# Kernel tuning notes

Measured on AMD Instinct MI355X. Metric: run time of the kernel, lower is better.

## Reference

```python
import jax, jax.numpy as jnp
import numpy as np

H = 2048      # hidden_size
NH = 16       # num_heads
HD = H // NH  # attention_head_size = 128
NEG_BIAS = -10000.0


def setup_inputs() -> dict:
    key = jax.random.key(0)
    k1, k2, k3, k4, k5 = jax.random.split(key, 5)
    B, S = 2, 2048
    hidden_states = jax.random.normal(k1, (B, S, H), dtype=jnp.float32)
    scale = 1.0 / np.sqrt(H)
    w_qkv = jax.random.normal(k2, (H, 3 * H), dtype=jnp.float32) * scale
    b_qkv = jax.random.normal(k3, (3 * H,), dtype=jnp.float32) * 0.01
    w_out = jax.random.normal(k4, (H, H), dtype=jnp.float32) * scale
    b_out = jax.random.normal(k5, (H,), dtype=jnp.float32) * 0.01
    return {"hidden_states": hidden_states, "w_qkv": w_qkv, "b_qkv": b_qkv,
            "w_out": w_out, "b_out": b_out}


def reference(hidden_states, w_qkv, b_qkv, w_out, b_out):
    B, S, _ = hidden_states.shape
    # fused QKV projection -> [B, S, 3H]
    qkv = hidden_states @ w_qkv + b_qkv
    # split heads with 3*head_dim per head, then chunk (matches torch code)
    qkv = qkv.reshape(B, S, NH, 3 * HD).transpose(0, 2, 1, 3)  # [B, NH, S, 3*HD]
    q, k, v = jnp.split(qkv, 3, axis=-1)                       # each [B, NH, S, HD]
    # scaled scores [B, NH, S, S]
    scores = jnp.einsum('bhqd,bhkd->bhqk', q, k) / np.sqrt(HD)
    causal = jnp.tril(jnp.ones((S, S), dtype=bool))
    scores = jnp.where(causal[None, None], scores, jnp.float32(NEG_BIAS))
    probs = jax.nn.softmax(scores, axis=-1)
    ctx = jnp.einsum('bhqk,bhkd->bhqd', probs, v)  # [B, NH, S, HD]
    ctx = ctx.transpose(0, 2, 1, 3).reshape(B, S, H)
    return ctx @ w_out + b_out
```

## Files before the change

kernel.cpp:

```cpp
#include <hip/hip_runtime.h>
#include <hip/hip_bf16.h>

typedef __bf16 bf16x8 __attribute__((ext_vector_type(8)));
typedef float  f32x4  __attribute__((ext_vector_type(4)));

constexpr int   Bb   = 2;
constexpr int   Slen = 2048;
constexpr int   Hdim = 2048;
constexpr int   NHn  = 16;
constexpr int   HDd  = 128;
constexpr int   LDP  = 136;
constexpr float QSCALE = 0.08838834764831845f;
constexpr float NEG    = -1e30f;

__device__ __forceinline__ void gld16(const __bf16* g, __bf16* l) {
    __builtin_amdgcn_global_load_lds(
        (__attribute__((address_space(1))) void*)(uintptr_t)(const void*)g,
        (__attribute__((address_space(3))) void*)l, 16, 0, 0);
}

__global__ __launch_bounds__(256) void cvt_bf16(const float* __restrict__ in,
                                                __bf16* __restrict__ out) {
    const size_t i = (size_t)(blockIdx.x * 256 + threadIdx.x) * 8;
    f32x4 a = *(const f32x4*)(in + i), b = *(const f32x4*)(in + i + 4);
    bf16x8 r;
    r[0] = (__bf16)a[0]; r[1] = (__bf16)a[1]; r[2] = (__bf16)a[2]; r[3] = (__bf16)a[3];
    r[4] = (__bf16)b[0]; r[5] = (__bf16)b[1]; r[6] = (__bf16)b[2]; r[7] = (__bf16)b[3];
    *(bf16x8*)(out + i) = r;
}

__global__ __launch_bounds__(256) void transpose_cvt(const float* __restrict__ in,
                                                     __bf16* __restrict__ out,
                                                     int R, int C) {
    __shared__ float t[64][65];
    const int c0 = blockIdx.x * 64, r0 = blockIdx.y * 64;
    const int tx = threadIdx.x & 63, ty = threadIdx.x >> 6;
#pragma unroll
    for (int i = 0; i < 16; ++i) {
        int r = i * 4 + ty;
        t[r][tx] = in[(size_t)(r0 + r) * C + c0 + tx];
    }
    __syncthreads();
#pragma unroll
    for (int i = 0; i < 16; ++i) {
        int r = i * 4 + ty;
        out[(size_t)(c0 + r) * R + r0 + tx] = (__bf16)t[tx][r];
    }
}


#define BAR    __builtin_amdgcn_s_barrier()
#define LGKM0  asm volatile("s_waitcnt lgkmcnt(0)" ::: "memory")
#define VMC(n) asm volatile("s_waitcnt vmcnt(" #n ")" ::: "memory")

#define STAGE(op, half, tt)                                                          \
  do {                                                                               \
    const int tt_ = (tt);                                                            \
    if (tt_ < NT) {                                                                  \
      __bf16* dst_ = lds + ((tt_ & 1) << 15) + ((op) << 14) + ((half) << 13);        \
      const __bf16* src_ = (op) ? Bt : A;                                            \
      const int rb_ = (op) ? n0 : m0;                                               \
      const int k0_ = tt_ << 6;                                                      \
      _Pragma("unroll")                                                              \
      for (int i_ = 0; i_ < 2; ++i_) {                                               \
        const int c_  = (i_ << 9) + tid;                                             \
        const int rl_ = c_ >> 3;                                                     \
        const int grow_ = rb_ + ((op) ? (((rl_ >> 5) << 6) + ((half) << 5) + (rl_ & 31)) \
                                      : (((rl_ >> 6) << 7) + ((half) << 6) + (rl_ & 63))); \
        const int gk_ = k0_ + (((c_ & 7) ^ (rl_ & 7)) << 3);                         \
        gld16(src_ + (size_t)grow_ * Kdim + gk_, dst_ + (c_ << 3));                  \
      }                                                                              \
    }                                                                                \
  } while (0)

#define LDA(bufv, mh)                                                                \
  do {                                                                               \
    const __bf16* Ab_ = lds + ((bufv) << 15) + ((mh) << 13) + (wg << 12) + (l16 << 6); \
    _Pragma("unroll")                                                                \
    for (int q_ = 0; q_ < 4; ++q_)                                                   \
      _Pragma("unroll")                                                              \
      for (int kk_ = 0; kk_ < 2; ++kk_)                                              \
        af[q_][kk_] = *(const bf16x8*)(Ab_ + (q_ << 10) +                            \
                        ((((kk_ << 2) + quad) ^ (l16 & 7)) << 3));                   \
  } while (0)

#define LDB(bufv, nh)                                                                \
  do {                                                                               \
    const __bf16* Bb_ = lds + ((bufv) << 15) + 16384 + ((nh) << 13) + (gn << 11) + (l16 << 6); \
    _Pragma("unroll")                                                                \
    for (int q_ = 0; q_ < 2; ++q_)                                                   \
      _Pragma("unroll")                                                              \
      for (int kk_ = 0; kk_ < 2; ++kk_)                                              \
        bfr[((nh) << 1) + q_][kk_] = *(const bf16x8*)(Bb_ + (q_ << 10) +             \
                        ((((kk_ << 2) + quad) ^ (l16 & 7)) << 3));                   \
  } while (0)

#define MM(mh, nh)                                                                   \
  do {                                                                               \
    _Pragma("unroll")                                                                \
    for (int q_ = 0; q_ < 4; ++q_)                                                   \
      _Pragma("unroll")                                                              \
      for (int n_ = 0; n_ < 2; ++n_)                                                 \
        _Pragma("unroll")                                                            \
        for (int kk_ = 0; kk_ < 2; ++kk_)                                            \
          acc[((mh) << 2) + q_][((nh) << 1) + n_] =                                  \
            __builtin_amdgcn_mfma_f32_16x16x32_bf16(                                 \
              af[q_][kk_], bfr[((nh) << 1) + n_][kk_],                               \
              acc[((mh) << 2) + q_][((nh) << 1) + n_], 0, 0, 0);                     \
  } while (0)

template <int MODE>
__global__ __launch_bounds__(512, 2) void gemm8(
    const __bf16* __restrict__ A, const __bf16* __restrict__ Bt,
    const float* __restrict__ bias, int Kdim, int Ndim,
    float* __restrict__ Cout,
    __bf16* __restrict__ Qo, __bf16* __restrict__ Ko, __bf16* __restrict__ Vto) {
    __shared__ __bf16 lds[65536];
    const int tid  = threadIdx.x;
    const int lane = tid & 63, wave = tid >> 6;
    const int quad = lane >> 4, l16 = lane & 15;
    const int wg = wave >> 2;
    const int gn = wave & 3;
    const int m0 = blockIdx.y * 256, n0 = blockIdx.x * 256;
    const int NT = Kdim >> 6;

    f32x4  acc[8][4] = {};
    bf16x8 af[4][2];
    bf16x8 bfr[4][2];

    STAGE(0, 0, 0); STAGE(1, 0, 0); STAGE(1, 1, 0); STAGE(0, 1, 0);
    STAGE(0, 0, 1); STAGE(1, 0, 1); STAGE(1, 1, 1);
    VMC(6);
    BAR;

    for (int t = 0; t < NT; ++t) {
        const int cb = t & 1;
        LDA(cb, 0); LDB(cb, 0);
        STAGE(0, 1, t + 1);
        BAR; LGKM0;
        __builtin_amdgcn_s_setprio(1); MM(0, 0); __builtin_amdgcn_s_setprio(0);
        BAR;
        LDB(cb, 1);
        STAGE(0, 0, t + 2);
        BAR; LGKM0;
        __builtin_amdgcn_s_setprio(1); MM(0, 1); __builtin_amdgcn_s_setprio(0);
        BAR;
        LDA(cb, 1);
        STAGE(1, 0, t + 2);
        BAR; LGKM0;
        __builtin_amdgcn_s_setprio(1); MM(1, 1); __builtin_amdgcn_s_setprio(0);
        BAR;
        STAGE(1, 1, t + 2);
        if (t < NT - 2) { VMC(6); } else { VMC(0); }
        BAR;
        __builtin_amdgcn_s_setprio(1); MM(1, 0); __builtin_amdgcn_s_setprio(0);
        BAR;
    }

#pragma unroll
    for (int mi = 0; mi < 8; ++mi) {
#pragma unroll
        for (int r = 0; r < 4; ++r) {
            const int m = m0 + wg * 128 + (mi >> 2) * 64 + (mi & 3) * 16 + quad * 4 + r;
            const int b = m >> 11, s = m & 2047;
#pragma unroll
            for (int ni = 0; ni < 4; ++ni) {
                const int cc = n0 + gn * 64 + (ni >> 1) * 32 + (ni & 1) * 16 + l16;
                float val = acc[mi][ni][r] + bias[cc];
                if (MODE == 1) {
                    Cout[(size_t)m * Ndim + cc] = val;
                } else {
                    const int h = cc / 384;
                    const int rr = cc - h * 384;
                    const size_t hb = ((size_t)(b * NHn + h) * Slen + s);
                    if (rr < 128)
                        Qo[hb * HDd + rr] = (__bf16)(val * QSCALE);
                    else if (rr < 256)
                        Ko[hb * HDd + (rr - 128)] = (__bf16)val;
                    else
                        Vto[((size_t)(b * NHn + h) * HDd + (rr - 256)) * Slen + s] = (__bf16)val;
                }
            }
        }
    }
}

__global__ __launch_bounds__(256) void attn_k(const __bf16* __restrict__ Q,
                                              const __bf16* __restrict__ Kmat,
                                              const __bf16* __restrict__ Vt,
                                              __bf16* __restrict__ ctx) {
    __shared__ __bf16 Ks[128 * LDP];
    __shared__ __bf16 Vs[128 * LDP];
    const int tid = threadIdx.x, lane = tid & 63, wave = tid >> 6;
    const int quad = lane >> 4, l16 = lane & 15;
    const int bh = blockIdx.y;
    const int qt = gridDim.x - 1 - blockIdx.x;
    const int b = bh >> 4, h = bh & 15;
    const __bf16* Qb = Q    + (size_t)bh * Slen * HDd;
    const __bf16* Kb = Kmat + (size_t)bh * Slen * HDd;
    const __bf16* Vb = Vt   + (size_t)bh * HDd * Slen;
    const int q0 = qt * 64;
    const int qa = q0 + wave * 16 + l16;
    const int qc = q0 + wave * 16 + quad * 4;

    bf16x8 qf[4];
#pragma unroll
    for (int kk = 0; kk < 4; ++kk)
        qf[kk] = *(const bf16x8*)(Qb + (size_t)qa * HDd + kk * 32 + quad * 8);

    f32x4 accO[8] = {};
    float m_i[4] = {NEG, NEG, NEG, NEG};
    float l_i[4] = {0.f, 0.f, 0.f, 0.f};

    const int ktiles = (q0 + 63) / 128 + 1;
    for (int kt = 0; kt < ktiles; ++kt) {
        const int kb0 = kt * 128;
        __syncthreads();
#pragma unroll
        for (int i = 0; i < 8; ++i) {
            int c = tid + i * 256;
            *(bf16x8*)(Ks + (c >> 4) * LDP + (c & 15) * 8) =
                *(const bf16x8*)(Kb + (size_t)(kb0 + (c >> 4)) * HDd + (c & 15) * 8);
            *(bf16x8*)(Vs + (c >> 4) * LDP + (c & 15) * 8) =
                *(const bf16x8*)(Vb + (size_t)(c >> 4) * Slen + kb0 + (c & 15) * 8);
        }
        __syncthreads();

        f32x4 sc[8];
#pragma unroll
        for (int nk = 0; nk < 8; ++nk) {
            f32x4 z = {0.f, 0.f, 0.f, 0.f};
#pragma unroll
            for (int kk = 0; kk < 4; ++kk) {
                bf16x8 kf = *(const bf16x8*)(Ks + (nk * 16 + l16) * LDP + kk * 32 + quad * 8);
                z = __builtin_amdgcn_mfma_f32_16x16x32_bf16(qf[kk], kf, z, 0, 0, 0);
            }
            sc[nk] = z;
        }
        if (kt == ktiles - 1) {
#pragma unroll
            for (int nk = 0; nk < 8; ++nk) {
                const int kg = kb0 + nk * 16 + l16;
#pragma unroll
                for (int r = 0; r < 4; ++r)
                    if (kg > qc + r) sc[nk][r] = NEG;
            }
        }
#pragma unroll
        for (int r = 0; r < 4; ++r) {
            float mm = sc[0][r];
#pragma unroll
            for (int nk = 1; nk < 8; ++nk) mm = fmaxf(mm, sc[nk][r]);
            mm = fmaxf(mm, __shfl_xor(mm, 1));
            mm = fmaxf(mm, __shfl_xor(mm, 2));
            mm = fmaxf(mm, __shfl_xor(mm, 4));
            mm = fmaxf(mm, __shfl_xor(mm, 8));
            const float mnew = fmaxf(m_i[r], mm);
            const float alpha = __expf(m_i[r] - mnew);
            float ls = 0.f;
#pragma unroll
            for (int nk = 0; nk < 8; ++nk) {
                float p = __expf(sc[nk][r] - mnew);
                sc[nk][r] = p;
                ls += p;
            }
            ls += __shfl_xor(ls, 1);
            ls += __shfl_xor(ls, 2);
            ls += __shfl_xor(ls, 4);
            ls += __shfl_xor(ls, 8);
            l_i[r] = l_i[r] * alpha + ls;
            m_i[r] = mnew;
#pragma unroll
            for (int nd = 0; nd < 8; ++nd) accO[nd][r] *= alpha;
        }

        __syncthreads();
        __bf16* Ps = Ks + wave * 16 * LDP;
#pragma unroll
        for (int nk = 0; nk < 8; ++nk)
#pragma unroll
            for (int r = 0; r < 4; ++r)
                Ps[(quad * 4 + r) * LDP + nk * 16 + l16] = (__bf16)sc[nk][r];
        __syncthreads();

        bf16x8 pf[4];
#pragma unroll
        for (int kk = 0; kk < 4; ++kk)
            pf[kk] = *(const bf16x8*)(Ps + l16 * LDP + kk * 32 + quad * 8);
#pragma unroll
        for (int nd = 0; nd < 8; ++nd)
#pragma unroll
            for (int kk = 0; kk < 4; ++kk) {
                bf16x8 vf = *(const bf16x8*)(Vs + (nd * 16 + l16) * LDP + kk * 32 + quad * 8);
                accO[nd] = __builtin_amdgcn_mfma_f32_16x16x32_bf16(pf[kk], vf, accO[nd], 0, 0, 0);
            }
    }

#pragma unroll
    for (int nd = 0; nd < 8; ++nd)
#pragma unroll
        for (int r = 0; r < 4; ++r) {
            const int s = q0 + wave * 16 + quad * 4 + r;
            const int d = nd * 16 + l16;
            const float o = accO[nd][r] / fmaxf(l_i[r], 1e-20f);
            ctx[((size_t)b * Slen + s) * Hdim + h * HDd + d] = (__bf16)o;
        }
}

extern "C" void kernel_launch(void* const* d_in, const int* in_sizes, int n_in,
                              void* d_out, int out_size, void* d_ws, size_t ws_size,
                              hipStream_t stream) {
    const float* hs   = (const float*)d_in[0];
    const float* wqkv = (const float*)d_in[1];
    const float* bqkv = (const float*)d_in[2];
    const float* wout = (const float*)d_in[3];
    const float* bout = (const float*)d_in[4];
    float* out = (float*)d_out;

    __bf16* ws    = (__bf16*)d_ws;
    __bf16* wqkvT = ws;
    __bf16* woutT = wqkvT + (size_t)6144 * 2048;
    __bf16* Qs    = woutT + (size_t)2048 * 2048;
    __bf16* Kms   = Qs  + (size_t)Bb * NHn * Slen * HDd;
    __bf16* Vts   = Kms + (size_t)Bb * NHn * Slen * HDd;
    __bf16* ctx   = Vts + (size_t)Bb * NHn * Slen * HDd;
    __bf16* hsb   = ctx;

    cvt_bf16<<<(Bb * Slen * Hdim) / (256 * 8), 256, 0, stream>>>(hs, hsb);
    transpose_cvt<<<dim3(6144 / 64, 2048 / 64), 256, 0, stream>>>(wqkv, wqkvT, 2048, 6144);
    transpose_cvt<<<dim3(2048 / 64, 2048 / 64), 256, 0, stream>>>(wout, woutT, 2048, 2048);
    gemm8<0><<<dim3(6144 / 256, 4096 / 256), 512, 0, stream>>>(
        hsb, wqkvT, bqkv, Hdim, 3 * Hdim, nullptr, Qs, Kms, Vts);
    attn_k<<<dim3(Slen / 64, Bb * NHn), 256, 0, stream>>>(Qs, Kms, Vts, ctx);
    gemm8<1><<<dim3(2048 / 256, 4096 / 256), 512, 0, stream>>>(
        ctx, woutT, bout, Hdim, Hdim, out, nullptr, nullptr, nullptr);
}
```

Measured before the change: 486.5 us.

## Double-buffer attention K/V tiles with async LDS loads and XOR swizzle

Reworks the attention kernel to use 128-query blocks with 8 waves and 64-key tiles. K and V tiles are double-buffered and loaded with direct global-to-LDS loads, so the next tile is fetched while the current one is computed. Padded LDS rows are replaced by an XOR swizzle, and each wave gets its own P buffer, which removes two block-wide barriers per tile. The cost is more LDS use per block, reliance on VMC/BAR/LGKM macros defined elsewhere, and the correctness of the swizzled indexing.

After: 477.9 us. No clear change (-1.8%).

```diff
diff --git a/kernel.cpp b/kernel.cpp
--- a/kernel.cpp
+++ b/kernel.cpp
@@ -9,7 +9,6 @@
 constexpr int   Hdim = 2048;
 constexpr int   NHn  = 16;
 constexpr int   HDd  = 128;
-constexpr int   LDP  = 136;
 constexpr float QSCALE = 0.08838834764831845f;
 constexpr float NEG    = -1e30f;
 
@@ -185,12 +184,34 @@
     }
 }
 
-__global__ __launch_bounds__(256) void attn_k(const __bf16* __restrict__ Q,
-                                              const __bf16* __restrict__ Kmat,
-                                              const __bf16* __restrict__ Vt,
-                                              __bf16* __restrict__ ctx) {
-    __shared__ __bf16 Ks[128 * LDP];
-    __shared__ __bf16 Vs[128 * LDP];
+
+#define ASTAGE(tt)                                                                   \
+  do {                                                                               \
+    const int tt_ = (tt);                                                            \
+    if (tt_ < ktiles) {                                                              \
+      const int kb_ = tt_ << 6;                                                      \
+      __bf16* kd_ = Ks + ((tt_ & 1) << 13);                                          \
+      __bf16* vd_ = Vs + ((tt_ & 1) << 13);                                          \
+      _Pragma("unroll")                                                              \
+      for (int i_ = 0; i_ < 2; ++i_) {                                               \
+        const int c_ = (i_ << 9) + tid;                        \
+        const int kr_ = c_ >> 4, kc_ = c_ & 15;           \
+        gld16(Kb + (size_t)(kb_ + kr_) * HDd + ((kc_ ^ (kr_ & 7)) << 3),             \
+              kd_ + (c_ << 3));                                                      \
+        const int vr_ = c_ >> 3, vc_ = c_ & 7;               \
+        gld16(Vb + (size_t)vr_ * Slen + kb_ + ((vc_ ^ (vr_ & 7)) << 3),              \
+              vd_ + (c_ << 3));                                                      \
+      }                                                                              \
+    }                                                                                \
+  } while (0)
+
+__global__ __launch_bounds__(512, 4) void attn_k(const __bf16* __restrict__ Q,
+                                                 const __bf16* __restrict__ Kmat,
+                                                 const __bf16* __restrict__ Vt,
+                                                 __bf16* __restrict__ ctx) {
+    __shared__ __bf16 Ks[2 * 64 * 128];
+    __shared__ __bf16 Vs[2 * 128 * 64];
+    __shared__ __bf16 Ps[8 * 16 * 64];
     const int tid = threadIdx.x, lane = tid & 63, wave = tid >> 6;
     const int quad = lane >> 4, l16 = lane & 15;
     const int bh = blockIdx.y;
@@ -199,9 +220,10 @@
     const __bf16* Qb = Q    + (size_t)bh * Slen * HDd;
     const __bf16* Kb = Kmat + (size_t)bh * Slen * HDd;
     const __bf16* Vb = Vt   + (size_t)bh * HDd * Slen;
-    const int q0 = qt * 64;
+    const int q0 = qt * 128;
     const int qa = q0 + wave * 16 + l16;
     const int qc = q0 + wave * 16 + quad * 4;
+    const int swz = (l16 & 7);
 
     bf16x8 qf[4];
 #pragma unroll
@@ -211,35 +233,36 @@
     f32x4 accO[8] = {};
     float m_i[4] = {NEG, NEG, NEG, NEG};
     float l_i[4] = {0.f, 0.f, 0.f, 0.f};
-
-    const int ktiles = (q0 + 63) / 128 + 1;
+    __bf16* Pw = Ps + wave * 1024;
+
+    const int ktiles = 2 * qt + 2;
+
+    ASTAGE(0);
     for (int kt = 0; kt < ktiles; ++kt) {
-        const int kb0 = kt * 128;
-        __syncthreads();
-#pragma unroll
-        for (int i = 0; i < 8; ++i) {
-            int c = tid + i * 256;
-            *(bf16x8*)(Ks + (c >> 4) * LDP + (c & 15) * 8) =
-                *(const bf16x8*)(Kb + (size_t)(kb0 + (c >> 4)) * HDd + (c & 15) * 8);
-            *(bf16x8*)(Vs + (c >> 4) * LDP + (c & 15) * 8) =
-                *(const bf16x8*)(Vb + (size_t)(c >> 4) * Slen + kb0 + (c & 15) * 8);
-        }
-        __syncthreads();
-
-        f32x4 sc[8];
-#pragma unroll
-        for (int nk = 0; nk < 8; ++nk) {
+        const int cur = kt & 1;
+        const int kb0 = kt * 64;
+        ASTAGE(kt + 1);
+        if (kt + 1 < ktiles) { VMC(4); } else { VMC(0); }
+        BAR;
+
+        const __bf16* Kt = Ks + (cur << 13);
+        const __bf16* Vc = Vs + (cur << 13);
+
+        f32x4 sc[4];
+#pragma unroll
+        for (int nk = 0; nk < 4; ++nk) {
             f32x4 z = {0.f, 0.f, 0.f, 0.f};
 #pragma unroll
             for (int kk = 0; kk < 4; ++kk) {
-                bf16x8 kf = *(const bf16x8*)(Ks + (nk * 16 + l16) * LDP + kk * 32 + quad * 8);
+                bf16x8 kf = *(const bf16x8*)(Kt + (nk * 16 + l16) * 128 +
+                                             (((kk << 2) + quad) ^ swz) * 8);
                 z = __builtin_amdgcn_mfma_f32_16x16x32_bf16(qf[kk], kf, z, 0, 0, 0);
             }
             sc[nk] = z;
         }
-        if (kt == ktiles - 1) {
-#pragma unroll
-            for (int nk = 0; nk < 8; ++nk) {
+        if (kt >= ktiles - 2) {
+#pragma unroll
+            for (int nk = 0; nk < 4; ++nk) {
                 const int kg = kb0 + nk * 16 + l16;
 #pragma unroll
                 for (int r = 0; r < 4; ++r)
@@ -248,9 +271,7 @@
         }
 #pragma unroll
         for (int r = 0; r < 4; ++r) {
-            float mm = sc[0][r];
-#pragma unroll
-            for (int nk = 1; nk < 8; ++nk) mm = fmaxf(mm, sc[nk][r]);
+            float mm = fmaxf(fmaxf(sc[0][r], sc[1][r]), fmaxf(sc[2][r], sc[3][r]));
             mm = fmaxf(mm, __shfl_xor(mm, 1));
             mm = fmaxf(mm, __shfl_xor(mm, 2));
             mm = fmaxf(mm, __shfl_xor(mm, 4));
@@ -259,7 +280,7 @@
             const float alpha = __expf(m_i[r] - mnew);
             float ls = 0.f;
 #pragma unroll
-            for (int nk = 0; nk < 8; ++nk) {
+            for (int nk = 0; nk < 4; ++nk) {
                 float p = __expf(sc[nk][r] - mnew);
                 sc[nk][r] = p;
                 ls += p;
@@ -274,26 +295,29 @@
             for (int nd = 0; nd < 8; ++nd) accO[nd][r] *= alpha;
         }
 
-        __syncthreads();
-        __bf16* Ps = Ks + wave * 16 * LDP;
-#pragma unroll
-        for (int nk = 0; nk < 8; ++nk)
-#pragma unroll
-            for (int r = 0; r < 4; ++r)
-                Ps[(quad * 4 + r) * LDP + nk * 16 + l16] = (__bf16)sc[nk][r];
-        __syncthreads();
-
-        bf16x8 pf[4];
-#pragma unroll
-        for (int kk = 0; kk < 4; ++kk)
-            pf[kk] = *(const bf16x8*)(Ps + l16 * LDP + kk * 32 + quad * 8);
+#pragma unroll
+        for (int nk = 0; nk < 4; ++nk)
+#pragma unroll
+            for (int r = 0; r < 4; ++r) {
+                const int row = quad * 4 + r, col = nk * 16 + l16;
+                Pw[row * 64 + (((col >> 3) ^ (row & 7)) << 3) + (col & 7)] =
+                    (__bf16)sc[nk][r];
+            }
+        bf16x8 pf[2];
+#pragma unroll
+        for (int kk = 0; kk < 2; ++kk)
+            pf[kk] = *(const bf16x8*)(Pw + l16 * 64 + ((((kk << 2) + quad) ^ swz) << 3));
+
 #pragma unroll
         for (int nd = 0; nd < 8; ++nd)
 #pragma unroll
-            for (int kk = 0; kk < 4; ++kk) {
-                bf16x8 vf = *(const bf16x8*)(Vs + (nd * 16 + l16) * LDP + kk * 32 + quad * 8);
+            for (int kk = 0; kk < 2; ++kk) {
+                bf16x8 vf = *(const bf16x8*)(Vc + (nd * 16 + l16) * 64 +
+                                             ((((kk << 2) + quad) ^ swz) << 3));
                 accO[nd] = __builtin_amdgcn_mfma_f32_16x16x32_bf16(pf[kk], vf, accO[nd], 0, 0, 0);
             }
+        LGKM0;
+        BAR;
     }
 
 #pragma unroll
@@ -331,7 +355,7 @@
     transpose_cvt<<<dim3(2048 / 64, 2048 / 64), 256, 0, stream>>>(wout, woutT, 2048, 2048);
     gemm8<0><<<dim3(6144 / 256, 4096 / 256), 512, 0, stream>>>(
         hsb, wqkvT, bqkv, Hdim, 3 * Hdim, nullptr, Qs, Kms, Vts);
-    attn_k<<<dim3(Slen / 64, Bb * NHn), 256, 0, stream>>>(Qs, Kms, Vts, ctx);
+    attn_k<<<dim3(Slen / 128, Bb * NHn), 512, 0, stream>>>(Qs, Kms, Vts, ctx);
     gemm8<1><<<dim3(2048 / 256, 4096 / 256), 512, 0, stream>>>(
         ctx, woutT, bout, Hdim, Hdim, out, nullptr, nullptr, nullptr);
 }
```
